# Performance work log

Measured on AMD Instinct MI355X. Metric: run time of the kernel, lower is better.

## Reference

```python
import jax, jax.numpy as jnp
import numpy as np

NUM_GRAPHS = 64

def _mlp(x, Wa, ba, Wb, bb):
    # 2-layer MLP: Linear -> ReLU -> Linear
    return jnp.maximum(x @ Wa + ba, 0.0) @ Wb + bb

def setup_inputs() -> dict:
    key = jax.random.key(0)
    ks = jax.random.split(key, 16)
    N1, E1, N2, E2 = 20000, 640000, 640000, 1280000
    d_x1, d_x2, d_e2, d_h, d_et, d_out = 32, 32, 16, 64, 32, 32
    inp = {
        'x1': jax.random.normal(ks[0], (N1, d_x1), jnp.float32),
        'x2': jax.random.normal(ks[1], (N2, d_x2), jnp.float32),
        'edge_index1': jax.random.randint(ks[2], (2, E1), 0, N1),
        'edge_index2': jax.random.randint(ks[3], (2, E2), 0, N2),
        'x1_batch': jnp.sort(jax.random.randint(ks[4], (N1,), 0, NUM_GRAPHS)),
        'edge_attr2': jax.random.normal(ks[5], (E2, d_e2), jnp.float32),
        # mlp2 (DGCN edge network): in = d_x2 + d_e2 = 48 -> 64 -> 32
        'W2a': jax.random.normal(ks[6], (d_x2 + d_e2, d_h), jnp.float32) * 0.05,
        'b2a': jnp.zeros((d_h,), jnp.float32),
        'W2b': jax.random.normal(ks[7], (d_h, d_et), jnp.float32) * 0.05,
        'b2b': jnp.zeros((d_et,), jnp.float32),
        # mlp (MOLGCN edge-conditioned network): in = d_x1 + d_et = 64 -> 64 -> 32
        'W1a': jax.random.normal(ks[8], (d_x1 + d_et, d_h), jnp.float32) * 0.05,
        'b1a': jnp.zeros((d_h,), jnp.float32),
        'W1b': jax.random.normal(ks[9], (d_h, d_out), jnp.float32) * 0.05,
        'b1b': jnp.zeros((d_out,), jnp.float32),
    }
    return inp

def reference(x1, x2, edge_index1, edge_index2, x1_batch, edge_attr2,
              W2a, b2a, W2b, b2b, W1a, b1a, W1b, b1b):
    N1, N2 = x1.shape[0], x2.shape[0]
    # --- DGCN over graph 2: message = mlp2([x_src, edge_attr]), sum-aggregate at dst ---
    s2, d2 = edge_index2[0], edge_index2[1]
    msg2 = _mlp(jnp.concatenate([x2[s2], edge_attr2], axis=-1), W2a, b2a, W2b, b2b)  # [E2, d_et]
    e_t = jax.ops.segment_sum(msg2, d2, num_segments=N2)  # [N2, d_et]; N2 == E1 (line graph)
    # --- MOLGCN over graph 1: edge-conditioned message = mlp([x_src, e_t]), sum at dst ---
    s1, d1 = edge_index1[0], edge_index1[1]
    msg1 = _mlp(jnp.concatenate([x1[s1], e_t], axis=-1), W1a, b1a, W1b, b1b)  # [E1, d_out]
    h = jax.ops.segment_sum(msg1, d1, num_segments=N1)  # [N1, d_out]
    # --- global add pool over graphs, then squeeze()/2 ---
    pooled = jax.ops.segment_sum(h, x1_batch, num_segments=NUM_GRAPHS)  # [G, d_out]
    return jnp.squeeze(pooled) / 2.0
```

## Files before the change

kernel.cpp:

```cpp
#include <hip/hip_runtime.h>
#include <hip/hip_bf16.h>


#define NUM_GRAPHS 64
#define CAP 4608
#define CURSTRIDE 16
#define EPB 8192

typedef __attribute__((ext_vector_type(8))) short bf16x8;
typedef __attribute__((ext_vector_type(4))) float f32x4;

__device__ __forceinline__ unsigned short f2bf(float x) {
    __hip_bfloat16 b = __float2bfloat16(x);
    return *(unsigned short*)&b;
}
__device__ __forceinline__ float bf2f(unsigned int u16) {
    unsigned short us = (unsigned short)u16;
    __hip_bfloat16 b = *(__hip_bfloat16*)&us;
    return __bfloat162float(b);
}
__device__ __forceinline__ unsigned int pack2(float lo, float hi) {
    return (unsigned int)f2bf(lo) | ((unsigned int)f2bf(hi) << 16);
}
__device__ __forceinline__ int swz(int row, int kb) {
    return row * 128 + (kb ^ ((row & 7) << 4));
}


__global__ __launch_bounds__(256) void k_prep0(
    const float* __restrict__ W2a, const float* __restrict__ b2a,
    const float* __restrict__ W2b, const float* __restrict__ b2b,
    const float* __restrict__ W1a, const float* __restrict__ b1a,
    const float* __restrict__ W1b, const float* __restrict__ b1b,
    unsigned char* __restrict__ wpack, int* __restrict__ cur, int ncur)
{
    const int tid = threadIdx.x;
    if (blockIdx.x == 0) {
        unsigned char* img1 = wpack;
        unsigned char* img2 = wpack + 12672;
        for (int i = tid; i < 64 * 64; i += 256) {
            int n = i >> 6, k = i & 63;
            float v1 = (k < 48) ? W2a[k * 64 + n] : 0.0f;
            *(unsigned short*)(img1 + n * 128 + ((2 * k) ^ ((n & 7) << 4))) = f2bf(v1);
            *(unsigned short*)(img2 + n * 128 + ((2 * k) ^ ((n & 7) << 4))) = f2bf(W1a[k * 64 + n]);
        }
        for (int i = tid; i < 32 * 64; i += 256) {
            int n = i >> 6, k = i & 63;
            *(unsigned short*)(img1 + 8192 + n * 128 + ((2 * k) ^ ((n & 7) << 4))) = f2bf(W2b[k * 32 + n]);
            *(unsigned short*)(img2 + 8192 + n * 128 + ((2 * k) ^ ((n & 7) << 4))) = f2bf(W1b[k * 32 + n]);
        }
        if (tid < 64) {
            ((float*)(img1 + 12288))[tid] = b2a[tid];
            ((float*)(img2 + 12288))[tid] = b1a[tid];
        }
        if (tid < 32) {
            ((float*)(img1 + 12544))[tid] = b2b[tid];
            ((float*)(img2 + 12544))[tid] = b1b[tid];
        }
    } else {
        for (int i = tid; i < ncur; i += 256) cur[i] = 0;
    }
}


__global__ __launch_bounds__(256) void k_cvt(
    const float* __restrict__ x2, uint4* __restrict__ x2b,
    const float* __restrict__ x1, uint4* __restrict__ x1b,
    long n2, long n1)
{
    const long tot = n2 + n1;
    const long stride = (long)gridDim.x * 256;
    for (long i = blockIdx.x * 256L + threadIdx.x; i < tot; i += stride) {
        const float* src = (i < n2) ? (x2 + i * 8) : (x1 + (i - n2) * 8);
        const float4* s4 = (const float4*)src;
        float4 a = s4[0], b = s4[1];
        uint4 o = make_uint4(pack2(a.x, a.y), pack2(a.z, a.w),
                             pack2(b.x, b.y), pack2(b.z, b.w));
        if (i < n2) x2b[i] = o; else x1b[i - n2] = o;
    }
}


__global__ __launch_bounds__(256) void k_bscat(
    const int* __restrict__ ei2, int E2, const int* __restrict__ ei1, int E1,
    int* __restrict__ cur, uint2* __restrict__ mid, int NB2, int NBT, int Etot)
{
    __shared__ unsigned int buck[EPB];
    __shared__ int hist[512];
    __shared__ int gbase[512];
    __shared__ int wloc[512];

    const int tid = threadIdx.x;
    const long start = (long)blockIdx.x * EPB;
    const int nloc = (int)(((long)Etot - start) < EPB ? ((long)Etot - start) : EPB);
    if (nloc <= 0) return;

    for (int i = tid; i < NBT; i += 256) hist[i] = 0;
    __syncthreads();

    for (int k = tid; k < nloc; k += 256) {
        const long i = start + k;
        int b, dlo;
        if (i < E2) {
            int d = ei2[E2 + i]; b = d >> 11; dlo = d & 2047;
        } else {
            int j = (int)(i - E2);
            int d = ei1[E1 + j]; b = NB2 + (d >> 7); dlo = d & 127;
        }
        buck[k] = (unsigned)b | ((unsigned)dlo << 16);
        atomicAdd(&hist[b], 1);
    }
    __syncthreads();

    for (int i = tid; i < NBT; i += 256) {
        const int c = hist[i];
        gbase[i] = (c > 0) ? atomicAdd(&cur[i * CURSTRIDE], c) : 0;
        wloc[i] = 0;
    }
    __syncthreads();

    for (int k = tid; k < nloc; k += 256) {
        const long i = start + k;
        const unsigned bv = buck[k];
        const int b = (int)(bv & 0xffffu), dlo = (int)(bv >> 16);
        int e, s;
        if (i < E2) { e = (int)i; s = ei2[i]; }
        else        { int j = (int)(i - E2); e = j; s = ei1[j]; }
        const int pos = gbase[b] + atomicAdd(&wloc[b], 1);
        if (pos < CAP)
            mid[(size_t)b * CAP + pos] =
                make_uint2((unsigned)e | ((unsigned)dlo << 21), (unsigned)s);
    }
}


__global__ __launch_bounds__(256) void k_csr(
    const int* __restrict__ cur, const uint2* __restrict__ mid,
    uint4* __restrict__ ord4, uint2* __restrict__ ord2,
    int NB2, int E2, int mode)
{
    __shared__ int cnt[2048];
    __shared__ int cnt2[2048];
    __shared__ int red[256];
    __shared__ int wpart[4];
    __shared__ int sCarry;

    const int b = blockIdx.x, tid = threadIdx.x;
    const bool g2 = (b < NB2);
    const int span = g2 ? 2048 : 128;
    const int node0 = g2 ? (b << 11) : ((b - NB2) << 7);
    const int lo = g2 ? 0 : NB2;
    const int fill = min(cur[b * CURSTRIDE], CAP);

    int part = 0;
    for (int k = lo + tid; k < b; k += 256) part += min(cur[k * CURSTRIDE], CAP);
    red[tid] = part;
    __syncthreads();
    for (int off = 128; off >= 1; off >>= 1) {
        if (tid < off) red[tid] += red[tid + off];
        __syncthreads();
    }
    const int outBase = (g2 ? 0 : E2) + red[0];

    for (int k = tid; k < span; k += 256) cnt[k] = 0;
    __syncthreads();

    const size_t mbase = (size_t)b * CAP;
    for (int i = tid; i < fill; i += 256)
        atomicAdd(&cnt[mid[mbase + i].x >> 21], 1);
    __syncthreads();

    if (tid == 0) sCarry = 0;
    __syncthreads();
    const int lane = tid & 63, wv = tid >> 6;
    for (int c0 = 0; c0 < span; c0 += 256) {
        const int idx = c0 + tid;
        int v = (idx < span) ? cnt[idx] : 0;
        int inc = v;
        #pragma unroll
        for (int off = 1; off < 64; off <<= 1) {
            int nv = __shfl_up(inc, off, 64);
            if (lane >= off) inc += nv;
        }
        if (lane == 63) wpart[wv] = inc;
        __syncthreads();
        int wpre = 0;
        for (int wq = 0; wq < wv; ++wq) wpre += wpart[wq];
        const int excl = sCarry + wpre + inc - v;
        const int tot = wpart[0] + wpart[1] + wpart[2] + wpart[3];
        __syncthreads();
        if (idx < span) cnt[idx] = excl;
        if (tid == 0) sCarry += tot;
        __syncthreads();
    }

    for (int k = tid; k < span; k += 256) cnt2[k] = 0;
    __syncthreads();

    for (int i = tid; i < fill; i += 256) {
        uint2 r = mid[mbase + i];
        const int dl = (int)(r.x >> 21);
        const int e = (int)(r.x & 0x1FFFFFu);
        const int rk = atomicAdd(&cnt2[dl], 1);
        const int o = outBase + cnt[dl] + rk;
        if (mode) ord4[o] = make_uint4((unsigned)e, r.y, (unsigned)(node0 + dl), 0u);
        else      ord2[o] = make_uint2((unsigned)e, (unsigned)(node0 + dl));
    }
}


__global__ __launch_bounds__(256) void k_msg2_agg(
    const float* __restrict__ x2f, const uint4* __restrict__ x2b,
    const float* __restrict__ ea2, const int* __restrict__ ei2,
    const uint4* __restrict__ ord4, const uint2* __restrict__ ord2,
    const unsigned char* __restrict__ wimg,
    unsigned int* __restrict__ e_t, int E, int mode, int use_bf16)
{
    __shared__ __align__(16) unsigned char sBuf[32768];
    __shared__ int sdst[257];
    __shared__ int sPrevS;
    __shared__ unsigned long long wmask[4];
    __shared__ int rstart[257];

    const int tid = threadIdx.x;
    const int base = blockIdx.x * 256, p = base + tid;

    int e = 0, s = 0, d = -1;
    if (p < E) {
        if (mode) { uint4 o = ord4[p]; e = (int)o.x; s = (int)o.y; d = (int)o.z; }
        else      { uint2 o = ord2[p]; e = (int)o.x; d = (int)o.y; s = ei2[e]; }
    }
    sdst[tid] = d;
    if (tid == 0) {
        int dp = -1, dn = -1;
        if (base > 0) dp = mode ? (int)ord4[base - 1].z : (int)ord2[base - 1].y;
        if (base + 256 < E) dn = mode ? (int)ord4[base + 256].z : (int)ord2[base + 256].y;
        sPrevS = dp; sdst[256] = dn;
    }

    {
        uint4 ch[8];
        if (use_bf16) {
            const uint4* xr = x2b + (size_t)s * 4;
            #pragma unroll
            for (int c = 0; c < 4; ++c) ch[c] = xr[c];
        } else {
            const float4* xs = (const float4*)(x2f + (size_t)s * 32);
            #pragma unroll
            for (int c = 0; c < 4; ++c) {
                float4 a = xs[2 * c], b = xs[2 * c + 1];
                ch[c].x = pack2(a.x, a.y); ch[c].y = pack2(a.z, a.w);
                ch[c].z = pack2(b.x, b.y); ch[c].w = pack2(b.z, b.w);
            }
        }
        const float4* es = (const float4*)(ea2 + (size_t)e * 16);
        #pragma unroll
        for (int c = 0; c < 2; ++c) {
            float4 a = es[2 * c], b = es[2 * c + 1];
            ch[4 + c].x = pack2(a.x, a.y); ch[4 + c].y = pack2(a.z, a.w);
            ch[4 + c].z = pack2(b.x, b.y); ch[4 + c].w = pack2(b.z, b.w);
        }
        ch[6] = make_uint4(0, 0, 0, 0);
        ch[7] = make_uint4(0, 0, 0, 0);
        #pragma unroll
        for (int c = 0; c < 8; ++c)
            *(uint4*)(sBuf + swz(tid, c * 16)) = ch[c];
    }
    __syncthreads();

    const int lane = tid & 63, wv = tid >> 6;
    const int lr = lane & 15, lk = lane >> 4;
    const int band = wv * 64;
    const unsigned char* gWa = wimg;
    const unsigned char* gWb = wimg + 8192;
    const float* gba = (const float*)(wimg + 12288);
    const float* gbb = (const float*)(wimg + 12544);

    f32x4 accA[4][4];
    #pragma unroll
    for (int n = 0; n < 4; ++n) {
        float bv = gba[n * 16 + lr];
        #pragma unroll
        for (int m = 0; m < 4; ++m) accA[m][n] = (f32x4){bv, bv, bv, bv};
    }
    #pragma unroll
    for (int ks = 0; ks < 2; ++ks) {
        const int kb = ks * 64 + lk * 16;
        bf16x8 af[4], bfr[4];
        #pragma unroll
        for (int m = 0; m < 4; ++m)
            af[m] = *(const bf16x8*)(sBuf + swz(band + m * 16 + lr, kb));
        #pragma unroll
        for (int n = 0; n < 4; ++n) {
            int rw = n * 16 + lr;
            bfr[n] = *(const bf16x8*)(gWa + rw * 128 + (kb ^ ((rw & 7) << 4)));
        }
        #pragma unroll
        for (int m = 0; m < 4; ++m)
            #pragma unroll
            for (int n = 0; n < 4; ++n)
                accA[m][n] = __builtin_amdgcn_mfma_f32_16x16x32_bf16(af[m], bfr[n], accA[m][n], 0, 0, 0);
    }
    #pragma unroll
    for (int m = 0; m < 4; ++m)
        #pragma unroll
        for (int n = 0; n < 4; ++n)
            #pragma unroll
            for (int rr = 0; rr < 4; ++rr) {
                int grow = band + m * 16 + lk * 4 + rr;
                int cb = 2 * (n * 16 + lr);
                *(unsigned short*)(sBuf + swz(grow, cb)) = f2bf(fmaxf(accA[m][n][rr], 0.0f));
            }

    f32x4 accB[4][2];
    #pragma unroll
    for (int n = 0; n < 2; ++n) {
        float bv = gbb[n * 16 + lr];
        #pragma unroll
        for (int m = 0; m < 4; ++m) accB[m][n] = (f32x4){bv, bv, bv, bv};
    }
    #pragma unroll
    for (int ks = 0; ks < 2; ++ks) {
        const int kb = ks * 64 + lk * 16;
        bf16x8 af[4], bfr[2];
        #pragma unroll
        for (int m = 0; m < 4; ++m)
            af[m] = *(const bf16x8*)(sBuf + swz(band + m * 16 + lr, kb));
        #pragma unroll
        for (int n = 0; n < 2; ++n) {
            int rw = n * 16 + lr;
            bfr[n] = *(const bf16x8*)(gWb + rw * 128 + (kb ^ ((rw & 7) << 4)));
        }
        #pragma unroll
        for (int m = 0; m < 4; ++m)
            #pragma unroll
            for (int n = 0; n < 2; ++n)
                accB[m][n] = __builtin_amdgcn_mfma_f32_16x16x32_bf16(af[m], bfr[n], accB[m][n], 0, 0, 0);
    }
    __syncthreads();

    unsigned short* smsg = (unsigned short*)sBuf;
    #pragma unroll
    for (int m = 0; m < 4; ++m)
        #pragma unroll
        for (int n = 0; n < 2; ++n)
            #pragma unroll
            for (int rr = 0; rr < 4; ++rr)
                smsg[(band + m * 16 + lk * 4 + rr) * 33 + n * 16 + lr] = f2bf(accB[m][n][rr]);

    const bool leader = (p < E) && (tid == 0 || sdst[tid - 1] != d);
    wmask[wv] = __ballot(leader);
    __syncthreads();

    int nruns = __popcll(wmask[0]) + __popcll(wmask[1]) + __popcll(wmask[2]) + __popcll(wmask[3]);
    if (leader) {
        int before = __popcll(wmask[wv] & ((1ULL << lane) - 1));
        for (int w = 0; w < wv; ++w) before += __popcll(wmask[w]);
        rstart[before] = tid;
    }
    const int vcnt = (E - base < 256) ? (E - base) : 256;
    if (tid == 0) rstart[nruns] = vcnt;
    __syncthreads();

    const int sPrev = sPrevS;
    const int ntask = nruns * 32;
    for (int task = tid; task < ntask; task += 256) {
        const int run = task >> 5, c = task & 31;
        const int rs = rstart[run], re = rstart[run + 1];
        const int dd = sdst[rs];
        float acc = 0.0f;
        for (int qq = rs; qq < re; ++qq) acc += bf2f(smsg[qq * 33 + c]);
        const bool gs = (rs > 0) || (base == 0) || (sPrev != dd);
        const bool ge = (re < 256) || (sdst[256] != dd);
        if (gs && ge) {
            ((unsigned short*)e_t)[(size_t)dd * 32 + c] = f2bf(acc);
        } else {
            unsigned int* a32 = e_t + (size_t)dd * 16 + (c >> 1);
            const int sh = (c & 1) * 16;
            unsigned int old = *a32;
            while (true) {
                float cur2 = bf2f((old >> sh) & 0xffffu);
                unsigned int nb = f2bf(cur2 + acc);
                unsigned int nv = (old & ~(0xffffu << sh)) | (nb << sh);
                unsigned int prev = atomicCAS(a32, old, nv);
                if (prev == old) break;
                old = prev;
            }
        }
    }
}


__global__ __launch_bounds__(256) void k_msg1_agg(
    const float* __restrict__ x1f, const uint4* __restrict__ x1b,
    const unsigned int* __restrict__ e_t, const int* __restrict__ ei1,
    const uint4* __restrict__ ord4, const uint2* __restrict__ ord2,
    const unsigned char* __restrict__ wimg,
    float* __restrict__ h, int E, int mode, int use_bf16)
{
    __shared__ __align__(16) unsigned char sBuf[32768];
    __shared__ int sdst[257];
    __shared__ int sPrevS;
    __shared__ unsigned long long wmask[4];
    __shared__ int rstart[257];

    const int tid = threadIdx.x;
    const int base = blockIdx.x * 256, p = base + tid;

    int e = 0, s = 0, d = -1;
    if (p < E) {
        if (mode) { uint4 o = ord4[p]; e = (int)o.x; s = (int)o.y; d = (int)o.z; }
        else      { uint2 o = ord2[p]; e = (int)o.x; d = (int)o.y; s = ei1[e]; }
    }
    sdst[tid] = d;
    if (tid == 0) {
        int dp = -1, dn = -1;
        if (base > 0) dp = mode ? (int)ord4[base - 1].z : (int)ord2[base - 1].y;
        if (base + 256 < E) dn = mode ? (int)ord4[base + 256].z : (int)ord2[base + 256].y;
        sPrevS = dp; sdst[256] = dn;
    }

    {
        uint4 ch[8];
        if (use_bf16) {
            const uint4* xr = x1b + (size_t)s * 4;
            #pragma unroll
            for (int c = 0; c < 4; ++c) ch[c] = xr[c];
        } else {
            const float4* xs = (const float4*)(x1f + (size_t)s * 32);
            #pragma unroll
            for (int c = 0; c < 4; ++c) {
                float4 a = xs[2 * c], b = xs[2 * c + 1];
                ch[c].x = pack2(a.x, a.y); ch[c].y = pack2(a.z, a.w);
                ch[c].z = pack2(b.x, b.y); ch[c].w = pack2(b.z, b.w);
            }
        }
        const uint4* er = (const uint4*)(e_t + (size_t)e * 16);
        #pragma unroll
        for (int c = 0; c < 4; ++c) ch[4 + c] = er[c];
        #pragma unroll
        for (int c = 0; c < 8; ++c)
            *(uint4*)(sBuf + swz(tid, c * 16)) = ch[c];
    }
    __syncthreads();

    const int lane = tid & 63, wv = tid >> 6;
    const int lr = lane & 15, lk = lane >> 4;
    const int band = wv * 64;
    const unsigned char* gWa = wimg;
    const unsigned char* gWb = wimg + 8192;
    const float* gba = (const float*)(wimg + 12288);
    const float* gbb = (const float*)(wimg + 12544);

    f32x4 accA[4][4];
    #pragma unroll
    for (int n = 0; n < 4; ++n) {
        float bv = gba[n * 16 + lr];
        #pragma unroll
        for (int m = 0; m < 4; ++m) accA[m][n] = (f32x4){bv, bv, bv, bv};
    }
    #pragma unroll
    for (int ks = 0; ks < 2; ++ks) {
        const int kb = ks * 64 + lk * 16;
        bf16x8 af[4], bfr[4];
        #pragma unroll
        for (int m = 0; m < 4; ++m)
            af[m] = *(const bf16x8*)(sBuf + swz(band + m * 16 + lr, kb));
        #pragma unroll
        for (int n = 0; n < 4; ++n) {
            int rw = n * 16 + lr;
            bfr[n] = *(const bf16x8*)(gWa + rw * 128 + (kb ^ ((rw & 7) << 4)));
        }
        #pragma unroll
        for (int m = 0; m < 4; ++m)
            #pragma unroll
            for (int n = 0; n < 4; ++n)
                accA[m][n] = __builtin_amdgcn_mfma_f32_16x16x32_bf16(af[m], bfr[n], accA[m][n], 0, 0, 0);
    }
    #pragma unroll
    for (int m = 0; m < 4; ++m)
        #pragma unroll
        for (int n = 0; n < 4; ++n)
            #pragma unroll
            for (int rr = 0; rr < 4; ++rr) {
                int grow = band + m * 16 + lk * 4 + rr;
                int cb = 2 * (n * 16 + lr);
                *(unsigned short*)(sBuf + swz(grow, cb)) = f2bf(fmaxf(accA[m][n][rr], 0.0f));
            }

    f32x4 accB[4][2];
    #pragma unroll
    for (int n = 0; n < 2; ++n) {
        float bv = gbb[n * 16 + lr];
        #pragma unroll
        for (int m = 0; m < 4; ++m) accB[m][n] = (f32x4){bv, bv, bv, bv};
    }
    #pragma unroll
    for (int ks = 0; ks < 2; ++ks) {
        const int kb = ks * 64 + lk * 16;
        bf16x8 af[4], bfr[2];
        #pragma unroll
        for (int m = 0; m < 4; ++m)
            af[m] = *(const bf16x8*)(sBuf + swz(band + m * 16 + lr, kb));
        #pragma unroll
        for (int n = 0; n < 2; ++n) {
            int rw = n * 16 + lr;
            bfr[n] = *(const bf16x8*)(gWb + rw * 128 + (kb ^ ((rw & 7) << 4)));
        }
        #pragma unroll
        for (int m = 0; m < 4; ++m)
            #pragma unroll
            for (int n = 0; n < 2; ++n)
                accB[m][n] = __builtin_amdgcn_mfma_f32_16x16x32_bf16(af[m], bfr[n], accB[m][n], 0, 0, 0);
    }
    __syncthreads();

    unsigned short* smsg = (unsigned short*)sBuf;
    #pragma unroll
    for (int m = 0; m < 4; ++m)
        #pragma unroll
        for (int n = 0; n < 2; ++n)
            #pragma unroll
            for (int rr = 0; rr < 4; ++rr)
                smsg[(band + m * 16 + lk * 4 + rr) * 33 + n * 16 + lr] = f2bf(accB[m][n][rr]);

    const bool leader = (p < E) && (tid == 0 || sdst[tid - 1] != d);
    wmask[wv] = __ballot(leader);
    __syncthreads();

    int nruns = __popcll(wmask[0]) + __popcll(wmask[1]) + __popcll(wmask[2]) + __popcll(wmask[3]);
    if (leader) {
        int before = __popcll(wmask[wv] & ((1ULL << lane) - 1));
        for (int w = 0; w < wv; ++w) before += __popcll(wmask[w]);
        rstart[before] = tid;
    }
    const int vcnt = (E - base < 256) ? (E - base) : 256;
    if (tid == 0) rstart[nruns] = vcnt;
    __syncthreads();

    const int sPrev = sPrevS;
    const int ntask = nruns * 32;
    for (int task = tid; task < ntask; task += 256) {
        const int run = task >> 5, c = task & 31;
        const int rs = rstart[run], re = rstart[run + 1];
        const int dd = sdst[rs];
        float acc = 0.0f;
        for (int qq = rs; qq < re; ++qq) acc += bf2f(smsg[qq * 33 + c]);
        const bool gs = (rs > 0) || (base == 0) || (sPrev != dd);
        const bool ge = (re < 256) || (sdst[256] != dd);
        if (gs && ge) h[(size_t)dd * 32 + c] = acc;
        else atomicAdd(h + (size_t)dd * 32 + c, acc);
    }
}


__device__ __forceinline__ int lower_bound_i(const int* a, int n, int key) {
    int lo = 0, hi = n;
    while (lo < hi) {
        int mid = (lo + hi) >> 1;
        if (a[mid] < key) lo = mid + 1; else hi = mid;
    }
    return lo;
}

__global__ __launch_bounds__(256) void k_pool(const float* __restrict__ h,
                                              const int* __restrict__ batch,
                                              float* __restrict__ out, int N1) {
    const int g = blockIdx.x;
    const int lo = lower_bound_i(batch, N1, g);
    const int hi = lower_bound_i(batch, N1, g + 1);
    const int tid = threadIdx.x;
    const int c = tid & 31, rg = tid >> 5;
    float acc = 0.0f;
    for (int n = lo + rg; n < hi; n += 8) acc += h[(size_t)n * 32 + c];
    __shared__ float red[256];
    red[tid] = acc;
    __syncthreads();
    for (int off = 128; off >= 32; off >>= 1) {
        if (tid < off) red[tid] += red[tid + off];
        __syncthreads();
    }
    if (tid < 32) out[g * 32 + tid] = red[tid] * 0.5f;
}


extern "C" void kernel_launch(void* const* d_in, const int* in_sizes, int n_in,
                              void* d_out, int out_size, void* d_ws, size_t ws_size,
                              hipStream_t stream) {
    const float* x1  = (const float*)d_in[0];
    const float* x2  = (const float*)d_in[1];
    const int*   ei1 = (const int*)d_in[2];
    const int*   ei2 = (const int*)d_in[3];
    const int*   xb  = (const int*)d_in[4];
    const float* ea2 = (const float*)d_in[5];
    const float* W2a = (const float*)d_in[6];
    const float* b2a = (const float*)d_in[7];
    const float* W2b = (const float*)d_in[8];
    const float* b2b = (const float*)d_in[9];
    const float* W1a = (const float*)d_in[10];
    const float* b1a = (const float*)d_in[11];
    const float* W1b = (const float*)d_in[12];
    const float* b1b = (const float*)d_in[13];

    const int N1 = in_sizes[0] / 32;
    const int E1 = in_sizes[2] / 2;
    const int E2 = in_sizes[3] / 2;
    const int N2 = in_sizes[1] / 32;
    const int Etot = E2 + E1;

    const int NB2 = (N2 + 2047) >> 11;
    const int NB1 = (N1 + 127) >> 7;
    const int NBT = NB2 + NB1;

    const size_t sz_wpack = 25600;
    const size_t sz_cur   = (size_t)NBT * CURSTRIDE * 4;
    const size_t sz_et    = (size_t)N2 * 64;
    const size_t sz_h     = (size_t)N1 * 128;
    const size_t sz_ord4  = (size_t)Etot * 16;
    const size_t sz_ord2  = (size_t)Etot * 8;
    const size_t sz_mid   = (size_t)NBT * CAP * 8;
    const size_t regA     = (sz_mid > sz_et + sz_h) ? sz_mid : (sz_et + sz_h);
    const size_t sz_x2b   = (size_t)N2 * 64;
    const size_t sz_x1b   = (size_t)N1 * 64;
    const size_t needA = sz_ord4 + regA + sz_x2b + sz_x1b + sz_wpack + sz_cur;

    const int mode = (ws_size >= needA) ? 1 : 0;
    const int use_bf16 = mode;

    char* w = (char*)d_ws;
    uint4* ord4 = (uint4*)w;
    uint2* ord2 = (uint2*)w;
    w += mode ? sz_ord4 : sz_ord2;
    char* regionA = w;                 w += regA;
    uint4* x2b = (uint4*)w;            if (mode) w += sz_x2b;
    uint4* x1b = (uint4*)w;            if (mode) w += sz_x1b;
    unsigned char* wpack = (unsigned char*)w;  w += sz_wpack;
    int* cur = (int*)w;

    unsigned int* e_t = (unsigned int*)regionA;
    float* h = (float*)(regionA + sz_et);
    uint2* mid = (uint2*)regionA;

    k_prep0<<<2, 256, 0, stream>>>(W2a, b2a, W2b, b2b, W1a, b1a, W1b, b1b,
                                   wpack, cur, NBT * CURSTRIDE);
    if (use_bf16)
        k_cvt<<<2048, 256, 0, stream>>>(x2, x2b, x1, x1b, (long)N2 * 4, (long)N1 * 4);
    k_bscat<<<(Etot + EPB - 1) / EPB, 256, 0, stream>>>(ei2, E2, ei1, E1, cur, mid, NB2, NBT, Etot);
    k_csr<<<NBT, 256, 0, stream>>>(cur, mid, ord4, ord2, NB2, E2, mode);
    hipMemsetAsync(regionA, 0, sz_et + sz_h, stream);
    k_msg2_agg<<<(E2 + 255) / 256, 256, 0, stream>>>(
        x2, x2b, ea2, ei2, ord4, ord2, wpack, e_t, E2, mode, use_bf16);
    k_msg1_agg<<<(E1 + 255) / 256, 256, 0, stream>>>(
        x1, x1b, e_t, ei1, ord4 + E2, ord2 + E2, wpack + 12672, h, E1, mode, use_bf16);
    k_pool<<<NUM_GRAPHS, 256, 0, stream>>>(h, xb, (float*)d_out, N1);
}
```

Before: 275.9 us.

## Compact edge order to 8 bytes, fuse conversion into bucket scatter, pre-convert edge_attr

The sorted edge order now uses a packed 8-byte record instead of 16 bytes. The destination is rebuilt from the bucket id, stored in the upper bits of the source field, plus the local offset. The bf16 conversion of x1/x2 is merged into the bucket-scatter kernel as extra blocks, which removes one launch and lets the conversion overlap the scatter. edge_attr2 is also pre-converted to bf16 so the message kernel reads half as many bytes. The costs are extra workspace and a bit-packing limit on node and bucket indices (20-bit source, 12-bit bucket).

```diff
diff --git a/kernel.cpp b/kernel.cpp
--- a/kernel.cpp
+++ b/kernel.cpp
@@ -6,6 +6,7 @@
 #define CAP 4608
 #define CURSTRIDE 16
 #define EPB 8192
+#define NCVT 2048
 
 typedef __attribute__((ext_vector_type(8))) short bf16x8;
 typedef __attribute__((ext_vector_type(4))) float f32x4;
@@ -21,6 +22,12 @@
 }
 __device__ __forceinline__ unsigned int pack2(float lo, float hi) {
     return (unsigned int)f2bf(lo) | ((unsigned int)f2bf(hi) << 16);
+}
+__device__ __forceinline__ uint4 cvt8(const float* src) {
+    const float4* s4 = (const float4*)src;
+    float4 a = s4[0], b = s4[1];
+    return make_uint4(pack2(a.x, a.y), pack2(a.z, a.w),
+                      pack2(b.x, b.y), pack2(b.z, b.w));
 }
 __device__ __forceinline__ int swz(int row, int kb) {
     return row * 128 + (kb ^ ((row & 7) << 4));
@@ -63,27 +70,13 @@
 }
 
 
-__global__ __launch_bounds__(256) void k_cvt(
+__global__ __launch_bounds__(256) void k_bscat_cvt(
+    const int* __restrict__ ei2, int E2, const int* __restrict__ ei1, int E1,
+    int* __restrict__ cur, uint2* __restrict__ mid, int NB2, int NBT, int Etot, int NBB,
     const float* __restrict__ x2, uint4* __restrict__ x2b,
     const float* __restrict__ x1, uint4* __restrict__ x1b,
-    long n2, long n1)
-{
-    const long tot = n2 + n1;
-    const long stride = (long)gridDim.x * 256;
-    for (long i = blockIdx.x * 256L + threadIdx.x; i < tot; i += stride) {
-        const float* src = (i < n2) ? (x2 + i * 8) : (x1 + (i - n2) * 8);
-        const float4* s4 = (const float4*)src;
-        float4 a = s4[0], b = s4[1];
-        uint4 o = make_uint4(pack2(a.x, a.y), pack2(a.z, a.w),
-                             pack2(b.x, b.y), pack2(b.z, b.w));
-        if (i < n2) x2b[i] = o; else x1b[i - n2] = o;
-    }
-}
-
-
-__global__ __launch_bounds__(256) void k_bscat(
-    const int* __restrict__ ei2, int E2, const int* __restrict__ ei1, int E1,
-    int* __restrict__ cur, uint2* __restrict__ mid, int NB2, int NBT, int Etot)
+    const float* __restrict__ ea2, uint4* __restrict__ ea2b,
+    long xn2, long xn1, long xne)
 {
     __shared__ unsigned int buck[EPB];
     __shared__ int hist[512];
@@ -91,6 +84,17 @@
     __shared__ int wloc[512];
 
     const int tid = threadIdx.x;
+    if (blockIdx.x >= NBB) {
+        const long tot = xn2 + xn1 + xne;
+        const long stride = (long)NCVT * 256;
+        for (long i = (long)(blockIdx.x - NBB) * 256 + tid; i < tot; i += stride) {
+            if (i < xn2) x2b[i] = cvt8(x2 + i * 8);
+            else if (i < xn2 + xn1) { long j = i - xn2; x1b[j] = cvt8(x1 + j * 8); }
+            else { long j = i - xn2 - xn1; ea2b[j] = cvt8(ea2 + j * 8); }
+        }
+        return;
+    }
+
     const long start = (long)blockIdx.x * EPB;
     const int nloc = (int)(((long)Etot - start) < EPB ? ((long)Etot - start) : EPB);
     if (nloc <= 0) return;
@@ -136,8 +140,7 @@
 
 __global__ __launch_bounds__(256) void k_csr(
     const int* __restrict__ cur, const uint2* __restrict__ mid,
-    uint4* __restrict__ ord4, uint2* __restrict__ ord2,
-    int NB2, int E2, int mode)
+    uint2* __restrict__ ord, int NB2, int E2)
 {
     __shared__ int cnt[2048];
     __shared__ int cnt2[2048];
@@ -148,7 +151,6 @@
     const int b = blockIdx.x, tid = threadIdx.x;
     const bool g2 = (b < NB2);
     const int span = g2 ? 2048 : 128;
-    const int node0 = g2 ? (b << 11) : ((b - NB2) << 7);
     const int lo = g2 ? 0 : NB2;
     const int fill = min(cur[b * CURSTRIDE], CAP);
 
@@ -200,21 +202,17 @@
     for (int i = tid; i < fill; i += 256) {
         uint2 r = mid[mbase + i];
         const int dl = (int)(r.x >> 21);
-        const int e = (int)(r.x & 0x1FFFFFu);
         const int rk = atomicAdd(&cnt2[dl], 1);
-        const int o = outBase + cnt[dl] + rk;
-        if (mode) ord4[o] = make_uint4((unsigned)e, r.y, (unsigned)(node0 + dl), 0u);
-        else      ord2[o] = make_uint2((unsigned)e, (unsigned)(node0 + dl));
+        ord[outBase + cnt[dl] + rk] = make_uint2(r.x, r.y | ((unsigned)b << 20));
     }
 }
 
 
 __global__ __launch_bounds__(256) void k_msg2_agg(
     const float* __restrict__ x2f, const uint4* __restrict__ x2b,
-    const float* __restrict__ ea2, const int* __restrict__ ei2,
-    const uint4* __restrict__ ord4, const uint2* __restrict__ ord2,
-    const unsigned char* __restrict__ wimg,
-    unsigned int* __restrict__ e_t, int E, int mode, int use_bf16)
+    const float* __restrict__ ea2, const uint4* __restrict__ ea2b,
+    const uint2* __restrict__ ord, const unsigned char* __restrict__ wimg,
+    unsigned int* __restrict__ e_t, int E, int use_bf16, int use_ea2b)
 {
     __shared__ __align__(16) unsigned char sBuf[32768];
     __shared__ int sdst[257];
@@ -227,14 +225,21 @@
 
     int e = 0, s = 0, d = -1;
     if (p < E) {
-        if (mode) { uint4 o = ord4[p]; e = (int)o.x; s = (int)o.y; d = (int)o.z; }
-        else      { uint2 o = ord2[p]; e = (int)o.x; d = (int)o.y; s = ei2[e]; }
+        uint2 o = ord[p];
+        e = (int)(o.x & 0x1FFFFFu); s = (int)(o.y & 0xFFFFFu);
+        d = ((int)(o.y >> 20) << 11) + (int)(o.x >> 21);
     }
     sdst[tid] = d;
     if (tid == 0) {
         int dp = -1, dn = -1;
-        if (base > 0) dp = mode ? (int)ord4[base - 1].z : (int)ord2[base - 1].y;
-        if (base + 256 < E) dn = mode ? (int)ord4[base + 256].z : (int)ord2[base + 256].y;
+        if (base > 0) {
+            uint2 o = ord[base - 1];
+            dp = ((int)(o.y >> 20) << 11) + (int)(o.x >> 21);
+        }
+        if (base + 256 < E) {
+            uint2 o = ord[base + 256];
+            dn = ((int)(o.y >> 20) << 11) + (int)(o.x >> 21);
+        }
         sPrevS = dp; sdst[256] = dn;
     }
 
@@ -253,12 +258,17 @@
                 ch[c].z = pack2(b.x, b.y); ch[c].w = pack2(b.z, b.w);
             }
         }
-        const float4* es = (const float4*)(ea2 + (size_t)e * 16);
-        #pragma unroll
-        for (int c = 0; c < 2; ++c) {
-            float4 a = es[2 * c], b = es[2 * c + 1];
-            ch[4 + c].x = pack2(a.x, a.y); ch[4 + c].y = pack2(a.z, a.w);
-            ch[4 + c].z = pack2(b.x, b.y); ch[4 + c].w = pack2(b.z, b.w);
+        if (use_ea2b) {
+            ch[4] = ea2b[(size_t)e * 2];
+            ch[5] = ea2b[(size_t)e * 2 + 1];
+        } else {
+            const float4* es = (const float4*)(ea2 + (size_t)e * 16);
+            #pragma unroll
+            for (int c = 0; c < 2; ++c) {
+                float4 a = es[2 * c], b = es[2 * c + 1];
+                ch[4 + c].x = pack2(a.x, a.y); ch[4 + c].y = pack2(a.z, a.w);
+                ch[4 + c].z = pack2(b.x, b.y); ch[4 + c].w = pack2(b.z, b.w);
+            }
         }
         ch[6] = make_uint4(0, 0, 0, 0);
         ch[7] = make_uint4(0, 0, 0, 0);
@@ -393,10 +403,9 @@
 
 __global__ __launch_bounds__(256) void k_msg1_agg(
     const float* __restrict__ x1f, const uint4* __restrict__ x1b,
-    const unsigned int* __restrict__ e_t, const int* __restrict__ ei1,
-    const uint4* __restrict__ ord4, const uint2* __restrict__ ord2,
-    const unsigned char* __restrict__ wimg,
-    float* __restrict__ h, int E, int mode, int use_bf16)
+    const unsigned int* __restrict__ e_t,
+    const uint2* __restrict__ ord, const unsigned char* __restrict__ wimg,
+    float* __restrict__ h, int E, int NB2, int use_bf16)
 {
     __shared__ __align__(16) unsigned char sBuf[32768];
     __shared__ int sdst[257];
@@ -409,14 +418,21 @@
 
     int e = 0, s = 0, d = -1;
     if (p < E) {
-        if (mode) { uint4 o = ord4[p]; e = (int)o.x; s = (int)o.y; d = (int)o.z; }
-        else      { uint2 o = ord2[p]; e = (int)o.x; d = (int)o.y; s = ei1[e]; }
+        uint2 o = ord[p];
+        e = (int)(o.x & 0x1FFFFFu); s = (int)(o.y & 0xFFFFFu);
+        d = (((int)(o.y >> 20) - NB2) << 7) + (int)(o.x >> 21);
     }
     sdst[tid] = d;
     if (tid == 0) {
         int dp = -1, dn = -1;
-        if (base > 0) dp = mode ? (int)ord4[base - 1].z : (int)ord2[base - 1].y;
-        if (base + 256 < E) dn = mode ? (int)ord4[base + 256].z : (int)ord2[base + 256].y;
+        if (base > 0) {
+            uint2 o = ord[base - 1];
+            dp = (((int)(o.y >> 20) - NB2) << 7) + (int)(o.x >> 21);
+        }
+        if (base + 256 < E) {
+            uint2 o = ord[base + 256];
+            dn = (((int)(o.y >> 20) - NB2) << 7) + (int)(o.x >> 21);
+        }
         sPrevS = dp; sdst[256] = dn;
     }
 
@@ -616,24 +632,24 @@
     const size_t sz_cur   = (size_t)NBT * CURSTRIDE * 4;
     const size_t sz_et    = (size_t)N2 * 64;
     const size_t sz_h     = (size_t)N1 * 128;
-    const size_t sz_ord4  = (size_t)Etot * 16;
-    const size_t sz_ord2  = (size_t)Etot * 8;
+    const size_t sz_ord   = (size_t)Etot * 8;
     const size_t sz_mid   = (size_t)NBT * CAP * 8;
     const size_t regA     = (sz_mid > sz_et + sz_h) ? sz_mid : (sz_et + sz_h);
     const size_t sz_x2b   = (size_t)N2 * 64;
     const size_t sz_x1b   = (size_t)N1 * 64;
-    const size_t needA = sz_ord4 + regA + sz_x2b + sz_x1b + sz_wpack + sz_cur;
-
-    const int mode = (ws_size >= needA) ? 1 : 0;
-    const int use_bf16 = mode;
+    const size_t sz_ea2b  = (size_t)E2 * 32;
+    const size_t need_x   = sz_ord + regA + sz_x2b + sz_x1b + sz_wpack + sz_cur;
+    const size_t need_xe  = need_x + sz_ea2b;
+
+    const int use_bf16 = (ws_size >= need_x) ? 1 : 0;
+    const int use_ea2b = (ws_size >= need_xe) ? 1 : 0;
 
     char* w = (char*)d_ws;
-    uint4* ord4 = (uint4*)w;
-    uint2* ord2 = (uint2*)w;
-    w += mode ? sz_ord4 : sz_ord2;
+    uint2* ord = (uint2*)w;            w += sz_ord;
     char* regionA = w;                 w += regA;
-    uint4* x2b = (uint4*)w;            if (mode) w += sz_x2b;
-    uint4* x1b = (uint4*)w;            if (mode) w += sz_x1b;
+    uint4* x2b = (uint4*)w;            if (use_bf16) w += sz_x2b;
+    uint4* x1b = (uint4*)w;            if (use_bf16) w += sz_x1b;
+    uint4* ea2b = (uint4*)w;           if (use_ea2b) w += sz_ea2b;
     unsigned char* wpack = (unsigned char*)w;  w += sz_wpack;
     int* cur = (int*)w;
 
@@ -641,16 +657,21 @@
     float* h = (float*)(regionA + sz_et);
     uint2* mid = (uint2*)regionA;
 
+    const int NBB = (Etot + EPB - 1) / EPB;
+    const long xn2 = use_bf16 ? (long)N2 * 4 : 0;
+    const long xn1 = use_bf16 ? (long)N1 * 4 : 0;
+    const long xne = use_ea2b ? (long)E2 * 2 : 0;
+
     k_prep0<<<2, 256, 0, stream>>>(W2a, b2a, W2b, b2b, W1a, b1a, W1b, b1b,
                                    wpack, cur, NBT * CURSTRIDE);
-    if (use_bf16)
-        k_cvt<<<2048, 256, 0, stream>>>(x2, x2b, x1, x1b, (long)N2 * 4, (long)N1 * 4);
-    k_bscat<<<(Etot + EPB - 1) / EPB, 256, 0, stream>>>(ei2, E2, ei1, E1, cur, mid, NB2, NBT, Etot);
-    k_csr<<<NBT, 256, 0, stream>>>(cur, mid, ord4, ord2, NB2, E2, mode);
+    k_bscat_cvt<<<NBB + NCVT, 256, 0, stream>>>(
+        ei2, E2, ei1, E1, cur, mid, NB2, NBT, Etot, NBB,
+        x2, x2b, x1, x1b, ea2, ea2b, xn2, xn1, xne);
+    k_csr<<<NBT, 256, 0, stream>>>(cur, mid, ord, NB2, E2);
     hipMemsetAsync(regionA, 0, sz_et + sz_h, stream);
     k_msg2_agg<<<(E2 + 255) / 256, 256, 0, stream>>>(
-        x2, x2b, ea2, ei2, ord4, ord2, wpack, e_t, E2, mode, use_bf16);
+        x2, x2b, ea2, ea2b, ord, wpack, e_t, E2, use_bf16, use_ea2b);
     k_msg1_agg<<<(E1 + 255) / 256, 256, 0, stream>>>(
-        x1, x1b, e_t, ei1, ord4 + E2, ord2 + E2, wpack + 12672, h, E1, mode, use_bf16);
+        x1, x1b, e_t, ord + E2, wpack + 12672, h, E1, NB2, use_bf16);
     k_pool<<<NUM_GRAPHS, 256, 0, stream>>>(h, xb, (float*)d_out, N1);
 }
```

Result: faster. 262.1 us (-5.0%).
